# Optimization experiments

Measured on AMD Instinct MI355X. Metric: run time of the kernel, lower is better.

The kernel has to match this reference:

```python
import jax, jax.numpy as jnp
import numpy as np

EPSILON = 1e-30

def compute_energy_density(F, lam, mu):
    # F: [E,3,3]; lam, mu: [E]
    C = jnp.einsum('...ji,...jk->...ik', F, F)
    J = jnp.linalg.det(F)
    Ic = C[..., 0, 0] + C[..., 1, 1] + C[..., 2, 2]
    delta = 1.0
    dim = 3
    alpha = (1.0 - 1.0 / (dim + delta)) * mu / lam + 1.0
    Ic_verified = jax.nn.relu(Ic + delta)
    return (mu / 2 * (Ic - dim)
            + lam / 2 * (J - alpha) ** 2
            - 0.5 * mu * jnp.log(Ic_verified + EPSILON))


def setup_inputs() -> dict:
    key = jax.random.key(0)
    ks = jax.random.split(key, 10)
    V, E = 8192, 40000
    next_position = jax.random.normal(ks[0], (V, 3), dtype=jnp.float32)
    position = jax.random.normal(ks[1], (V, 3), dtype=jnp.float32)
    velocity = jax.random.normal(ks[2], (V, 3), dtype=jnp.float32) * 0.1
    external_acceleration = jax.random.normal(ks[3], (V, 3), dtype=jnp.float32) * 0.1
    int_density_matrix = jax.random.uniform(ks[4], (V, V), dtype=jnp.float32)
    elements = jax.random.randint(ks[5], (E, 4), 0, V, dtype=jnp.int64)
    polynomials = jax.random.normal(ks[6], (E, 4, 4), dtype=jnp.float32)
    measure = jax.random.uniform(ks[7], (E, 4, 1), dtype=jnp.float32)
    lam = jax.random.uniform(ks[8], (E,), dtype=jnp.float32) + 1.0  # keep away from 0 (divided by in alpha)
    mu = jax.random.uniform(ks[9], (E,), dtype=jnp.float32) + 0.5
    time_step = jnp.ones((), dtype=jnp.float32)
    return {"next_position": next_position, "position": position, "velocity": velocity,
            "external_acceleration": external_acceleration, "int_density_matrix": int_density_matrix,
            "elements": elements, "polynomials": polynomials, "measure": measure,
            "lam": lam, "mu": mu, "time_step": time_step}


def reference(next_position, position, velocity, external_acceleration,
              int_density_matrix, elements, polynomials, measure, lam, mu, time_step):
    inv_h = 1.0 / time_step
    coefficient = inv_h ** 2 / 2
    # Kinetic term: einsum('ij,ji->', M, delta @ delta.T) == sum(delta * (M @ delta))
    # (avoids materializing the [V,V] delta @ delta.T intermediate)
    y = position + velocity * time_step + external_acceleration * time_step ** 2
    delta = next_position - y  # [V,3]
    kinetic_energy = coefficient * jnp.sum(delta * (int_density_matrix @ delta))
    # Elastic term: gather element vertex positions, build deformation gradient F
    basis_derivatives_q = polynomials[:, :4, :3]          # [E,4,3]
    local_position = next_position[elements]               # [E,4,3] gather
    F = jnp.einsum('bft,bfl->btl', local_position, basis_derivatives_q)  # [E,3,3]
    psi = compute_energy_density(F, lam, mu)               # [E]
    elastic_energy = jnp.einsum('b,b->', psi, measure[:, 3, 0])
    energy = kinetic_energy + elastic_energy
    return energy, kinetic_energy, elastic_energy
```

## Files before the change

### kernel.cpp

```cpp
#include <hip/hip_runtime.h>

#define V 8192
#define RPW 2
#define KBLOCKS (V / (RPW * 4))

__global__ __launch_bounds__(256) void prep_kernel(
    const float* __restrict__ next_pos, const float* __restrict__ pos,
    const float* __restrict__ vel, const float* __restrict__ ext,
    const float* __restrict__ dt_p, float* __restrict__ ws) {
  int i = blockIdx.x * blockDim.x + threadIdx.x;
  if (i < 2) ws[i] = 0.f;
  if (i < V) {
    float dt = dt_p[0];
    float dt2 = dt * dt;
    float* dx = ws + 16;
    float* dy = dx + V;
    float* dz = dy + V;
    dx[i] = next_pos[3*i+0] - (pos[3*i+0] + vel[3*i+0]*dt + ext[3*i+0]*dt2);
    dy[i] = next_pos[3*i+1] - (pos[3*i+1] + vel[3*i+1]*dt + ext[3*i+1]*dt2);
    dz[i] = next_pos[3*i+2] - (pos[3*i+2] + vel[3*i+2]*dt + ext[3*i+2]*dt2);
  }
}

__global__ __launch_bounds__(256) void kinetic_kernel(
    const float* __restrict__ M, const float* __restrict__ dsoa,
    float* __restrict__ acc) {
  const float* __restrict__ dx = dsoa;
  const float* __restrict__ dy = dsoa + V;
  const float* __restrict__ dz = dsoa + 2 * V;
  const float4* __restrict__ dx4 = (const float4*)dx;
  const float4* __restrict__ dy4 = (const float4*)dy;
  const float4* __restrict__ dz4 = (const float4*)dz;

  const int t = threadIdx.x;
  const int lane = t & 63;
  const int wv = t >> 6;
  const int wave = blockIdx.x * 4 + wv;
  const int r0 = wave * RPW;

  float rx[RPW], ry[RPW], rz[RPW];
#pragma unroll
  for (int r = 0; r < RPW; ++r) {
    rx[r] = dx[r0 + r];
    ry[r] = dy[r0 + r];
    rz[r] = dz[r0 + r];
  }

  float a = 0.f;
#pragma unroll 2
  for (int i = 0; i < V / 4 / 64; ++i) {
    const int k = i * 64 + lane;
    const float4 cx = dx4[k];
    const float4 cy = dy4[k];
    const float4 cz = dz4[k];
#pragma unroll
    for (int r = 0; r < RPW; ++r) {
      const float4 m = *(const float4*)(M + (size_t)(r0 + r) * V + 4 * k);
      a += m.x * (rx[r]*cx.x + ry[r]*cy.x + rz[r]*cz.x);
      a += m.y * (rx[r]*cx.y + ry[r]*cy.y + rz[r]*cz.y);
      a += m.z * (rx[r]*cx.z + ry[r]*cy.z + rz[r]*cz.z);
      a += m.w * (rx[r]*cx.w + ry[r]*cy.w + rz[r]*cz.w);
    }
  }

#pragma unroll
  for (int off = 32; off; off >>= 1) a += __shfl_down(a, off, 64);

  __shared__ float lds[4];
  if (lane == 0) lds[wv] = a;
  __syncthreads();
  if (t == 0) atomicAdd(acc, lds[0] + lds[1] + lds[2] + lds[3]);
}

__global__ __launch_bounds__(256) void elastic_kernel(
    const float* __restrict__ next_pos, const int* __restrict__ elements,
    const float* __restrict__ poly, const float* __restrict__ measure,
    const float* __restrict__ lam, const float* __restrict__ mu,
    float* __restrict__ acc, int E) {
  int e = blockIdx.x * blockDim.x + threadIdx.x;
  float contrib = 0.f;
  if (e < E) {
    float F00 = 0.f, F01 = 0.f, F02 = 0.f;
    float F10 = 0.f, F11 = 0.f, F12 = 0.f;
    float F20 = 0.f, F21 = 0.f, F22 = 0.f;
#pragma unroll
    for (int f = 0; f < 4; ++f) {
      int vi = elements[e * 4 + f];
      const float* p = next_pos + 3 * (size_t)vi;
      float px = p[0], py = p[1], pz = p[2];
      const float* b = poly + (size_t)e * 16 + f * 4;
      float b0 = b[0], b1 = b[1], b2 = b[2];
      F00 += px * b0; F01 += px * b1; F02 += px * b2;
      F10 += py * b0; F11 += py * b1; F12 += py * b2;
      F20 += pz * b0; F21 += pz * b1; F22 += pz * b2;
    }
    float Ic = F00*F00 + F01*F01 + F02*F02 +
               F10*F10 + F11*F11 + F12*F12 +
               F20*F20 + F21*F21 + F22*F22;
    float J = F00 * (F11 * F22 - F12 * F21)
            - F01 * (F10 * F22 - F12 * F20)
            + F02 * (F10 * F21 - F11 * F20);
    float l = lam[e], m = mu[e];
    float alpha = 0.75f * m / l + 1.f;
    float Icv = fmaxf(Ic + 1.f, 0.f);
    float d = J - alpha;
    float psi = 0.5f * m * (Ic - 3.f) + 0.5f * l * d * d
              - 0.5f * m * logf(Icv + 1e-30f);
    contrib = psi * measure[e * 4 + 3];
  }
#pragma unroll
  for (int off = 32; off; off >>= 1) contrib += __shfl_down(contrib, off, 64);
  __shared__ float w[4];
  int lane = threadIdx.x & 63, wv = threadIdx.x >> 6;
  if (lane == 0) w[wv] = contrib;
  __syncthreads();
  if (threadIdx.x == 0) atomicAdd(acc, w[0] + w[1] + w[2] + w[3]);
}

__global__ void finalize_kernel(const float* __restrict__ ws,
                                const float* __restrict__ dt_p,
                                float* __restrict__ out) {
  float dt = dt_p[0];
  float inv_h = 1.f / dt;
  float coeff = 0.5f * inv_h * inv_h;
  float kin = coeff * ws[0];
  float ela = ws[1];
  out[0] = kin + ela;
  out[1] = kin;
  out[2] = ela;
}

extern "C" void kernel_launch(void* const* d_in, const int* in_sizes, int n_in,
                              void* d_out, int out_size, void* d_ws, size_t ws_size,
                              hipStream_t stream) {
  const float* next_pos = (const float*)d_in[0];
  const float* pos      = (const float*)d_in[1];
  const float* vel      = (const float*)d_in[2];
  const float* ext      = (const float*)d_in[3];
  const float* M        = (const float*)d_in[4];
  const int*   elements = (const int*)d_in[5];
  const float* poly     = (const float*)d_in[6];
  const float* measure  = (const float*)d_in[7];
  const float* lam      = (const float*)d_in[8];
  const float* mu       = (const float*)d_in[9];
  const float* dt_p     = (const float*)d_in[10];
  float* out = (float*)d_out;
  float* ws  = (float*)d_ws;
  const int E = in_sizes[5] / 4;

  prep_kernel<<<(V + 255) / 256, 256, 0, stream>>>(next_pos, pos, vel, ext, dt_p, ws);
  kinetic_kernel<<<KBLOCKS, 256, 0, stream>>>(M, ws + 16, ws);
  elastic_kernel<<<(E + 255) / 256, 256, 0, stream>>>(next_pos, elements, poly,
                                                      measure, lam, mu, ws + 1, E);
  finalize_kernel<<<1, 1, 0, stream>>>(ws, dt_p, out);
}
```

Measured before the change: 384.6 us.

## Fuse elastic, kinetic and finalize kernels into one with last-block finalize

Merges the elastic-energy computation into the front of the kinetic GEMV kernel, so the first ceil(E/256) blocks do the elastic work before streaming their rows of M. Finalization now happens in whichever block finishes last, detected with an atomic done-counter and a thread fence, which removes two kernel launches. The cost is that some blocks carry extra elastic work, which may unbalance the bandwidth-bound pass over M. The kernel also assumes E fits within KBLOCKS*256 elements; larger E would leave elements uncomputed.

```diff
diff --git a/kernel.cpp b/kernel.cpp
--- a/kernel.cpp
+++ b/kernel.cpp
@@ -9,7 +9,7 @@
     const float* __restrict__ vel, const float* __restrict__ ext,
     const float* __restrict__ dt_p, float* __restrict__ ws) {
   int i = blockIdx.x * blockDim.x + threadIdx.x;
-  if (i < 2) ws[i] = 0.f;
+  if (i < 3) ws[i] = 0.f;
   if (i < V) {
     float dt = dt_p[0];
     float dt2 = dt * dt;
@@ -22,19 +22,64 @@
   }
 }
 
-__global__ __launch_bounds__(256) void kinetic_kernel(
-    const float* __restrict__ M, const float* __restrict__ dsoa,
-    float* __restrict__ acc) {
-  const float* __restrict__ dx = dsoa;
-  const float* __restrict__ dy = dsoa + V;
-  const float* __restrict__ dz = dsoa + 2 * V;
+__global__ __launch_bounds__(256, 4) void main_kernel(
+    const float* __restrict__ M, const float* __restrict__ next_pos,
+    const int* __restrict__ elements, const float* __restrict__ poly,
+    const float* __restrict__ measure, const float* __restrict__ lam,
+    const float* __restrict__ mu, const float* __restrict__ dt_p,
+    float* __restrict__ ws, float* __restrict__ out, int E) {
+  const int t = threadIdx.x;
+  const int lane = t & 63;
+  const int wv = t >> 6;
+  __shared__ float red[4];
+
+  if ((int)blockIdx.x * 256 < E) {
+    int e = blockIdx.x * 256 + t;
+    float contrib = 0.f;
+    if (e < E) {
+      float F00 = 0.f, F01 = 0.f, F02 = 0.f;
+      float F10 = 0.f, F11 = 0.f, F12 = 0.f;
+      float F20 = 0.f, F21 = 0.f, F22 = 0.f;
+#pragma unroll
+      for (int f = 0; f < 4; ++f) {
+        int vi = elements[e * 4 + f];
+        const float* p = next_pos + 3 * (size_t)vi;
+        float px = p[0], py = p[1], pz = p[2];
+        const float* b = poly + (size_t)e * 16 + f * 4;
+        float b0 = b[0], b1 = b[1], b2 = b[2];
+        F00 += px * b0; F01 += px * b1; F02 += px * b2;
+        F10 += py * b0; F11 += py * b1; F12 += py * b2;
+        F20 += pz * b0; F21 += pz * b1; F22 += pz * b2;
+      }
+      float Ic = F00*F00 + F01*F01 + F02*F02 +
+                 F10*F10 + F11*F11 + F12*F12 +
+                 F20*F20 + F21*F21 + F22*F22;
+      float J = F00 * (F11 * F22 - F12 * F21)
+              - F01 * (F10 * F22 - F12 * F20)
+              + F02 * (F10 * F21 - F11 * F20);
+      float l = lam[e], m = mu[e];
+      float alpha = 0.75f * m / l + 1.f;
+      float Icv = fmaxf(Ic + 1.f, 0.f);
+      float d = J - alpha;
+      float psi = 0.5f * m * (Ic - 3.f) + 0.5f * l * d * d
+                - 0.5f * m * logf(Icv + 1e-30f);
+      contrib = psi * measure[e * 4 + 3];
+    }
+#pragma unroll
+    for (int off = 32; off; off >>= 1) contrib += __shfl_down(contrib, off, 64);
+    if (lane == 0) red[wv] = contrib;
+    __syncthreads();
+    if (t == 0) atomicAdd(ws + 1, red[0] + red[1] + red[2] + red[3]);
+    __syncthreads();
+  }
+
+  const float* __restrict__ dx = ws + 16;
+  const float* __restrict__ dy = dx + V;
+  const float* __restrict__ dz = dy + V;
   const float4* __restrict__ dx4 = (const float4*)dx;
   const float4* __restrict__ dy4 = (const float4*)dy;
   const float4* __restrict__ dz4 = (const float4*)dz;
 
-  const int t = threadIdx.x;
-  const int lane = t & 63;
-  const int wv = t >> 6;
   const int wave = blockIdx.x * 4 + wv;
   const int r0 = wave * RPW;
 
@@ -65,69 +110,25 @@
 
 #pragma unroll
   for (int off = 32; off; off >>= 1) a += __shfl_down(a, off, 64);
+  if (lane == 0) red[wv] = a;
+  __syncthreads();
 
-  __shared__ float lds[4];
-  if (lane == 0) lds[wv] = a;
-  __syncthreads();
-  if (t == 0) atomicAdd(acc, lds[0] + lds[1] + lds[2] + lds[3]);
-}
-
-__global__ __launch_bounds__(256) void elastic_kernel(
-    const float* __restrict__ next_pos, const int* __restrict__ elements,
-    const float* __restrict__ poly, const float* __restrict__ measure,
-    const float* __restrict__ lam, const float* __restrict__ mu,
-    float* __restrict__ acc, int E) {
-  int e = blockIdx.x * blockDim.x + threadIdx.x;
-  float contrib = 0.f;
-  if (e < E) {
-    float F00 = 0.f, F01 = 0.f, F02 = 0.f;
-    float F10 = 0.f, F11 = 0.f, F12 = 0.f;
-    float F20 = 0.f, F21 = 0.f, F22 = 0.f;
-#pragma unroll
-    for (int f = 0; f < 4; ++f) {
-      int vi = elements[e * 4 + f];
-      const float* p = next_pos + 3 * (size_t)vi;
-      float px = p[0], py = p[1], pz = p[2];
-      const float* b = poly + (size_t)e * 16 + f * 4;
-      float b0 = b[0], b1 = b[1], b2 = b[2];
-      F00 += px * b0; F01 += px * b1; F02 += px * b2;
-      F10 += py * b0; F11 += py * b1; F12 += py * b2;
-      F20 += pz * b0; F21 += pz * b1; F22 += pz * b2;
+  if (t == 0) {
+    atomicAdd(ws + 0, red[0] + red[1] + red[2] + red[3]);
+    __threadfence();
+    unsigned done = atomicAdd((unsigned*)(ws + 2), 1u);
+    if (done == gridDim.x - 1) {
+      float kin_raw = atomicAdd(ws + 0, 0.f);
+      float ela     = atomicAdd(ws + 1, 0.f);
+      float dt = dt_p[0];
+      float inv_h = 1.f / dt;
+      float coeff = 0.5f * inv_h * inv_h;
+      float kin = coeff * kin_raw;
+      out[0] = kin + ela;
+      out[1] = kin;
+      out[2] = ela;
     }
-    float Ic = F00*F00 + F01*F01 + F02*F02 +
-               F10*F10 + F11*F11 + F12*F12 +
-               F20*F20 + F21*F21 + F22*F22;
-    float J = F00 * (F11 * F22 - F12 * F21)
-            - F01 * (F10 * F22 - F12 * F20)
-            + F02 * (F10 * F21 - F11 * F20);
-    float l = lam[e], m = mu[e];
-    float alpha = 0.75f * m / l + 1.f;
-    float Icv = fmaxf(Ic + 1.f, 0.f);
-    float d = J - alpha;
-    float psi = 0.5f * m * (Ic - 3.f) + 0.5f * l * d * d
-              - 0.5f * m * logf(Icv + 1e-30f);
-    contrib = psi * measure[e * 4 + 3];
   }
-#pragma unroll
-  for (int off = 32; off; off >>= 1) contrib += __shfl_down(contrib, off, 64);
-  __shared__ float w[4];
-  int lane = threadIdx.x & 63, wv = threadIdx.x >> 6;
-  if (lane == 0) w[wv] = contrib;
-  __syncthreads();
-  if (threadIdx.x == 0) atomicAdd(acc, w[0] + w[1] + w[2] + w[3]);
-}
-
-__global__ void finalize_kernel(const float* __restrict__ ws,
-                                const float* __restrict__ dt_p,
-                                float* __restrict__ out) {
-  float dt = dt_p[0];
-  float inv_h = 1.f / dt;
-  float coeff = 0.5f * inv_h * inv_h;
-  float kin = coeff * ws[0];
-  float ela = ws[1];
-  out[0] = kin + ela;
-  out[1] = kin;
-  out[2] = ela;
 }
 
 extern "C" void kernel_launch(void* const* d_in, const int* in_sizes, int n_in,
@@ -149,8 +150,6 @@
   const int E = in_sizes[5] / 4;
 
   prep_kernel<<<(V + 255) / 256, 256, 0, stream>>>(next_pos, pos, vel, ext, dt_p, ws);
-  kinetic_kernel<<<KBLOCKS, 256, 0, stream>>>(M, ws + 16, ws);
-  elastic_kernel<<<(E + 255) / 256, 256, 0, stream>>>(next_pos, elements, poly,
-                                                      measure, lam, mu, ws + 1, E);
-  finalize_kernel<<<1, 1, 0, stream>>>(ws, dt_p, out);
+  main_kernel<<<KBLOCKS, 256, 0, stream>>>(M, next_pos, elements, poly, measure,
+                                           lam, mu, dt_p, ws, out, E);
 }
```

New measurement: 433.2 us. 12.6% more time.

## Split kinetic columns across wave pairs and fuse finalize into elastic kernel

Applied to the files above, without the earlier changes.

The kinetic matvec now assigns each pair of waves the same two rows, with each wave covering half of the columns. This doubles the block count, giving more parallelism and memory-level concurrency across CUs. The separate finalize launch is removed: the elastic kernel uses an atomic completion counter so the last block writes the outputs. This trades one kernel launch for extra atomics and a threadfence per block. The counter is stored as an unsigned value in a float workspace slot.

```diff
diff --git a/kernel.cpp b/kernel.cpp
--- a/kernel.cpp
+++ b/kernel.cpp
@@ -2,14 +2,15 @@
 
 #define V 8192
 #define RPW 2
-#define KBLOCKS (V / (RPW * 4))
+#define CSPLIT 2
+#define KBLOCKS (V * CSPLIT / (RPW * 4))
 
 __global__ __launch_bounds__(256) void prep_kernel(
     const float* __restrict__ next_pos, const float* __restrict__ pos,
     const float* __restrict__ vel, const float* __restrict__ ext,
     const float* __restrict__ dt_p, float* __restrict__ ws) {
   int i = blockIdx.x * blockDim.x + threadIdx.x;
-  if (i < 2) ws[i] = 0.f;
+  if (i < 3) ws[i] = 0.f;
   if (i < V) {
     float dt = dt_p[0];
     float dt2 = dt * dt;
@@ -36,7 +37,8 @@
   const int lane = t & 63;
   const int wv = t >> 6;
   const int wave = blockIdx.x * 4 + wv;
-  const int r0 = wave * RPW;
+  const int r0 = (wave >> 1) * RPW;
+  const int kbase = (wave & 1) * (V / 4 / CSPLIT);
 
   float rx[RPW], ry[RPW], rz[RPW];
 #pragma unroll
@@ -48,8 +50,8 @@
 
   float a = 0.f;
 #pragma unroll 2
-  for (int i = 0; i < V / 4 / 64; ++i) {
-    const int k = i * 64 + lane;
+  for (int i = 0; i < V / 4 / 64 / CSPLIT; ++i) {
+    const int k = kbase + i * 64 + lane;
     const float4 cx = dx4[k];
     const float4 cy = dy4[k];
     const float4 cz = dz4[k];
@@ -76,7 +78,8 @@
     const float* __restrict__ next_pos, const int* __restrict__ elements,
     const float* __restrict__ poly, const float* __restrict__ measure,
     const float* __restrict__ lam, const float* __restrict__ mu,
-    float* __restrict__ acc, int E) {
+    const float* __restrict__ dt_p, float* __restrict__ ws,
+    float* __restrict__ out, int E) {
   int e = blockIdx.x * blockDim.x + threadIdx.x;
   float contrib = 0.f;
   if (e < E) {
@@ -114,20 +117,22 @@
   int lane = threadIdx.x & 63, wv = threadIdx.x >> 6;
   if (lane == 0) w[wv] = contrib;
   __syncthreads();
-  if (threadIdx.x == 0) atomicAdd(acc, w[0] + w[1] + w[2] + w[3]);
-}
-
-__global__ void finalize_kernel(const float* __restrict__ ws,
-                                const float* __restrict__ dt_p,
-                                float* __restrict__ out) {
-  float dt = dt_p[0];
-  float inv_h = 1.f / dt;
-  float coeff = 0.5f * inv_h * inv_h;
-  float kin = coeff * ws[0];
-  float ela = ws[1];
-  out[0] = kin + ela;
-  out[1] = kin;
-  out[2] = ela;
+  if (threadIdx.x == 0) {
+    atomicAdd(ws + 1, w[0] + w[1] + w[2] + w[3]);
+    __threadfence();
+    unsigned done = atomicAdd((unsigned*)(ws + 2), 1u);
+    if (done == gridDim.x - 1) {
+      float ela     = atomicAdd(ws + 1, 0.f);
+      float kin_raw = atomicAdd(ws + 0, 0.f);
+      float dt = dt_p[0];
+      float inv_h = 1.f / dt;
+      float coeff = 0.5f * inv_h * inv_h;
+      float kin = coeff * kin_raw;
+      out[0] = kin + ela;
+      out[1] = kin;
+      out[2] = ela;
+    }
+  }
 }
 
 extern "C" void kernel_launch(void* const* d_in, const int* in_sizes, int n_in,
@@ -151,6 +156,6 @@
   prep_kernel<<<(V + 255) / 256, 256, 0, stream>>>(next_pos, pos, vel, ext, dt_p, ws);
   kinetic_kernel<<<KBLOCKS, 256, 0, stream>>>(M, ws + 16, ws);
   elastic_kernel<<<(E + 255) / 256, 256, 0, stream>>>(next_pos, elements, poly,
-                                                      measure, lam, mu, ws + 1, E);
-  finalize_kernel<<<1, 1, 0, stream>>>(ws, dt_p, out);
+                                                      measure, lam, mu, dt_p,
+                                                      ws, out, E);
 }
```

Result: slower. 408.3 us (+6.1%).
